# Optimization experiments

Hardware: AMD Instinct MI355X
Metric: run time of the kernel (lower is better)

## Reference

```python
import jax, jax.numpy as jnp
import numpy as np

N = 100000   # nodes
E = 1600000  # edges (avg in-degree 16)
IN, H, C = 128, 128, 40
K = 2        # TAGConv hops (DGL default)


def setup_inputs() -> dict:
    key = jax.random.key(0)
    ks = jax.random.split(key, 7)
    in_feat = jax.random.normal(ks[0], (N, IN), dtype=jnp.float32)
    src = jax.random.randint(ks[1], (E,), 0, N)
    dst = jax.random.randint(ks[2], (E,), 0, N)
    # TAGConv linear: concat of (K+1) hop features -> out
    W1 = jax.random.normal(ks[3], ((K + 1) * IN, H), dtype=jnp.float32) / np.float32(np.sqrt((K + 1) * IN))
    b1 = jnp.zeros((H,), dtype=jnp.float32)
    W2 = jax.random.normal(ks[4], ((K + 1) * H, C), dtype=jnp.float32) / np.float32(np.sqrt((K + 1) * H))
    b2 = jnp.zeros((C,), dtype=jnp.float32)
    return {"in_feat": in_feat, "src": src, "dst": dst,
            "W1": W1, "b1": b1, "W2": W2, "b2": b2}


def _tagconv(x, src, dst, norm, W, b):
    feats = [x]
    h = x
    for _ in range(K):
        h = norm[:, None] * h                               # [N, d]
        h = jax.ops.segment_sum(h[src], dst, num_segments=N)  # SpMM via gather+scatter
        h = norm[:, None] * h
        feats.append(h)
    return jnp.concatenate(feats, axis=-1) @ W + b


def reference(in_feat, src, dst, W1, b1, W2, b2):
    deg = jax.ops.segment_sum(jnp.ones((E,), jnp.float32), dst, num_segments=N)
    norm = jnp.where(deg > 0, deg ** -0.5, 0.0)             # D^{-1/2}, inf -> 0
    h = jax.nn.relu(_tagconv(in_feat, src, dst, norm, W1, b1))
    h = jax.nn.relu(_tagconv(h, src, dst, norm, W2, b2))
    return jnp.mean(h, axis=0, keepdims=True)               # dgl.mean_nodes -> [1, C]
```

## Files before the change

kernel.cpp:

```cpp
#include <hip/hip_runtime.h>

typedef unsigned short u16;
typedef __attribute__((ext_vector_type(8))) short bf16x8;
typedef __attribute__((ext_vector_type(4))) float f32x4;

#define CSR_CHUNK 12288

__device__ inline u16 f2bf(float f) {
    union { float f; unsigned u; } v; v.f = f;
    unsigned r = v.u + 0x7fff + ((v.u >> 16) & 1);
    return (u16)(r >> 16);
}
__device__ inline float bflo(unsigned u) {
    union { unsigned u; float f; } v; v.u = u << 16; return v.f;
}
__device__ inline float bfhi(unsigned u) {
    union { unsigned u; float f; } v; v.u = u & 0xffff0000u; return v.f;
}
__device__ inline float bfs(u16 x) { return bflo((unsigned)x); }
__device__ inline unsigned pk(float lo, float hi) {
    return (unsigned)f2bf(lo) | ((unsigned)f2bf(hi) << 16);
}

__global__ __launch_bounds__(256) void prep_k(
    const float* __restrict__ X, u16* __restrict__ Xb, long n4,
    const float* __restrict__ W1, u16* __restrict__ Wp1,
    const float* __restrict__ W2, u16* __restrict__ Wp2,
    int* __restrict__ bcnt, int nzero) {
    int b = blockIdx.x;
    int t = threadIdx.x;
    if (b < 4) {
        int i = b * 256 + t;
        if (i < nzero) bcnt[i] = 0;
        return;
    }
    b -= 4;
    if (b < 192) {
        int i = b * 256 + t;
        int m = i >> 14, r = i & 16383;
        int jj = r & 7, lane = (r >> 3) & 63, kk = (r >> 9) & 3, tt = r >> 11;
        int k = kk * 32 + (lane >> 4) * 8 + jj;
        int c = tt * 16 + (lane & 15);
        Wp1[i] = f2bf(W1[(size_t)m * 16384 + k * 128 + c]);
        return;
    }
    b -= 192;
    if (b < 64) {
        int i = b * 256 + t;
        int jj = i & 7, lane = (i >> 3) & 63, kk = (i >> 9) & 3, tt = i >> 11;
        int k = kk * 32 + (lane >> 4) * 8 + jj;
        int c = tt * 16 + (lane & 15);
        float v = 0.f;
        if (c < 120) {
            int hop = c / 40, j = c - hop * 40;
            v = W2[(size_t)(hop * 128 + k) * 40 + j];
        }
        Wp2[i] = f2bf(v);
        return;
    }
    b -= 64;
    long i = (long)b * 256 + t;
    if (i >= n4) return;
    float4 v = ((const float4*)X)[i];
    ushort4 o;
    o.x = f2bf(v.x); o.y = f2bf(v.y); o.z = f2bf(v.z); o.w = f2bf(v.w);
    ((ushort4*)Xb)[i] = o;
}

__global__ __launch_bounds__(256) void bucket_cnt_k(
    const int* __restrict__ dst, int* __restrict__ bcnt, int E, int nbuck) {
    __shared__ int hist[1024];
    int e0 = blockIdx.x * CSR_CHUNK;
    int e1 = min(e0 + CSR_CHUNK, E);
    for (int i = threadIdx.x; i < nbuck; i += 256) hist[i] = 0;
    __syncthreads();
    for (int e = e0 + threadIdx.x; e < e1; e += 256)
        atomicAdd(&hist[dst[e] >> 7], 1);
    __syncthreads();
    for (int i = threadIdx.x; i < nbuck; i += 256) {
        int c = hist[i];
        if (c) atomicAdd(&bcnt[i], c);
    }
}

__global__ void bscan_k(const int* __restrict__ bcnt, int* __restrict__ bptr,
                        int* __restrict__ bcur, int nb, int E) {
    __shared__ int lds[256];
    int t = threadIdx.x;
    int base = t * 4;
    int v[4];
    int s = 0;
#pragma unroll
    for (int i = 0; i < 4; ++i) {
        v[i] = s;
        int idx = base + i;
        s += (idx < nb) ? bcnt[idx] : 0;
    }
    int x = s;
    lds[t] = x;
    __syncthreads();
    for (int off = 1; off < 256; off <<= 1) {
        int y = (t >= off) ? lds[t - off] : 0;
        __syncthreads();
        x += y;
        lds[t] = x;
        __syncthreads();
    }
    int toff = x - s;
#pragma unroll
    for (int i = 0; i < 4; ++i) {
        int idx = base + i;
        if (idx < nb) {
            int e0 = toff + v[i];
            bptr[idx] = e0;
            bcur[idx] = e0;
        }
    }
    if (t == 255) bptr[nb] = E;
}

__global__ __launch_bounds__(256) void passB_k(
    const int* __restrict__ src, const int* __restrict__ dst,
    int* __restrict__ bcur, int2* __restrict__ tmp, int E, int nbuck) {
    __shared__ int hist[1024];
    __shared__ int bbase[1024];
    int e0 = blockIdx.x * CSR_CHUNK;
    int e1 = min(e0 + CSR_CHUNK, E);
    for (int i = threadIdx.x; i < nbuck; i += 256) hist[i] = 0;
    __syncthreads();
    for (int e = e0 + threadIdx.x; e < e1; e += 256)
        atomicAdd(&hist[dst[e] >> 7], 1);
    __syncthreads();
    for (int i = threadIdx.x; i < nbuck; i += 256) {
        int c = hist[i];
        bbase[i] = c ? atomicAdd(&bcur[i], c) : 0;
        hist[i] = 0;
    }
    __syncthreads();
    for (int e = e0 + threadIdx.x; e < e1; e += 256) {
        int s = src[e], d = dst[e];
        int b = d >> 7;
        int r = atomicAdd(&hist[b], 1);
        int2 sd; sd.x = s; sd.y = d;
        tmp[bbase[b] + r] = sd;
    }
}

__global__ __launch_bounds__(256) void passC_k(
    const int2* __restrict__ tmp, const int* __restrict__ bptr,
    int* __restrict__ rowptr, float* __restrict__ norm, int* __restrict__ esrc,
    int N, int E) {
    __shared__ int cnt[128];
    __shared__ int sc[128];
    __shared__ int cur[128];
    int b = blockIdx.x, t = threadIdx.x;
    int base = bptr[b], endp = bptr[b + 1];
    int node0 = b << 7;
    int nNodes = min(128, N - node0);

    if (t < 128) cnt[t] = 0;
    __syncthreads();
    for (int i = base + t; i < endp; i += 256)
        atomicAdd(&cnt[tmp[i].y & 127], 1);
    __syncthreads();
    if (t < 128) sc[t] = cnt[t];
    __syncthreads();
    for (int off = 1; off < 128; off <<= 1) {
        int y = 0;
        if (t < 128 && t >= off) y = sc[t - off];
        __syncthreads();
        if (t < 128) sc[t] += y;
        __syncthreads();
    }
    if (t < 128) {
        int ex = sc[t] - cnt[t];
        cur[t] = ex;
        if (t < nNodes) {
            rowptr[node0 + t] = base + ex;
            int d = cnt[t];
            norm[node0 + t] = (d > 0) ? rsqrtf((float)d) : 0.f;
        }
    }
    if (b == gridDim.x - 1 && t == 0) rowptr[N] = E;
    __syncthreads();
    for (int i = base + t; i < endp; i += 256) {
        int2 sd = tmp[i];
        int pos = atomicAdd(&cur[sd.y & 127], 1);
        esrc[base + pos] = sd.x;
    }
}

template <int MODE>
__global__ __launch_bounds__(256, 2) void gemm_mfma_k(
    const u16* __restrict__ Ab, const u16* __restrict__ Wp,
    float* __restrict__ Cf, u16* __restrict__ Cb,
    float* __restrict__ Cf2, u16* __restrict__ Cb2,
    const float* __restrict__ norm, int n, int nStripes) {
    int lane = threadIdx.x & 63;
    int wave = threadIdx.x >> 6;
    int rit = lane & 15;
    int kgrp = lane >> 4;

    bf16x8 bfr[8][4];
    const bf16x8* wp = (const bf16x8*)Wp;
#pragma unroll
    for (int t = 0; t < 8; ++t)
#pragma unroll
        for (int kk = 0; kk < 4; ++kk)
            bfr[t][kk] = wp[(t * 4 + kk) * 64 + lane];

    for (int s = blockIdx.x; s < nStripes; s += gridDim.x) {
        int r0 = s * 64 + wave * 16;
        int ar = min(r0 + rit, n - 1);
        const bf16x8* arow = (const bf16x8*)(Ab + (size_t)ar * 128);
        bf16x8 afr[4];
#pragma unroll
        for (int kk = 0; kk < 4; ++kk) afr[kk] = arow[kk * 4 + kgrp];

        f32x4 acc[8];
#pragma unroll
        for (int t = 0; t < 8; ++t) acc[t] = (f32x4)(0.f);
#pragma unroll
        for (int kk = 0; kk < 4; ++kk)
#pragma unroll
            for (int t = 0; t < 8; ++t)
                acc[t] = __builtin_amdgcn_mfma_f32_16x16x32_bf16(
                    afr[kk], bfr[t][kk], acc[t], 0, 0, 0);

#pragma unroll
        for (int j = 0; j < 4; ++j) {
            int rs = r0 + kgrp * 4 + j;
            if (rs >= n) continue;
            float nr = (MODE == 4) ? 0.f : norm[rs];
#pragma unroll
            for (int t = 0; t < 8; ++t) {
                int c = t * 16 + rit;
                float v = acc[t][j];
                if (MODE == 0) {
                    if (c < 40) Cf[(size_t)rs * 40 + c] = v;
                    else if (c < 80) Cf2[(size_t)rs * 40 + c - 40] = v;
                    else if (c < 120) Cb2[(size_t)rs * 40 + c - 80] = f2bf(v * nr);
                } else if (MODE == 1) {
                    Cb[(size_t)rs * 128 + c] = f2bf(v * nr);
                } else {
                    Cb[(size_t)rs * 128 + c] = f2bf(v);
                }
            }
        }
    }
}

template <int F>
__global__ __launch_bounds__(256) void spmm128_f_k(
    const u16* __restrict__ g, const u16* __restrict__ P,
    const float* __restrict__ bias, u16* __restrict__ outb,
    const float* __restrict__ norm,
    const int* __restrict__ rowptr, const int* __restrict__ esrc, int n) {
    int node = (blockIdx.x * 256 + threadIdx.x) >> 6;
    if (node >= n) return;
    int lane = threadIdx.x & 63;
    int sub = lane >> 4;
    int l16 = lane & 15;
    int beg = rowptr[node], end = rowptr[node + 1];
    float a[8];
#pragma unroll
    for (int j = 0; j < 8; ++j) a[j] = 0.f;

    int e = beg + sub;
    for (; e + 4 < end; e += 8) {
        int s0 = esrc[e], s1 = esrc[e + 4];
        uint4 v0 = *(const uint4*)(g + (size_t)s0 * 128 + l16 * 8);
        uint4 v1 = *(const uint4*)(g + (size_t)s1 * 128 + l16 * 8);
        a[0] += bflo(v0.x); a[1] += bfhi(v0.x);
        a[2] += bflo(v0.y); a[3] += bfhi(v0.y);
        a[4] += bflo(v0.z); a[5] += bfhi(v0.z);
        a[6] += bflo(v0.w); a[7] += bfhi(v0.w);
        a[0] += bflo(v1.x); a[1] += bfhi(v1.x);
        a[2] += bflo(v1.y); a[3] += bfhi(v1.y);
        a[4] += bflo(v1.z); a[5] += bfhi(v1.z);
        a[6] += bflo(v1.w); a[7] += bfhi(v1.w);
    }
    for (; e < end; e += 4) {
        int s = esrc[e];
        uint4 v = *(const uint4*)(g + (size_t)s * 128 + l16 * 8);
        a[0] += bflo(v.x); a[1] += bfhi(v.x);
        a[2] += bflo(v.y); a[3] += bfhi(v.y);
        a[4] += bflo(v.z); a[5] += bfhi(v.z);
        a[6] += bflo(v.w); a[7] += bfhi(v.w);
    }
#pragma unroll
    for (int j = 0; j < 8; ++j) {
        a[j] += __shfl_xor(a[j], 16);
        a[j] += __shfl_xor(a[j], 32);
    }
    if (sub == 0) {
        float nn = norm[node];
        uint4 pv = *(const uint4*)(P + (size_t)node * 128 + l16 * 8);
        float p[8];
        p[0] = bflo(pv.x); p[1] = bfhi(pv.x);
        p[2] = bflo(pv.y); p[3] = bfhi(pv.y);
        p[4] = bflo(pv.z); p[5] = bfhi(pv.z);
        p[6] = bflo(pv.w); p[7] = bfhi(pv.w);
        float r[8];
        if (F == 1) {
#pragma unroll
            for (int j = 0; j < 8; ++j) r[j] = nn * (p[j] + nn * a[j]);
        } else {
            float4 b0 = *(const float4*)(bias + l16 * 8);
            float4 b1v = *(const float4*)(bias + l16 * 8 + 4);
            r[0] = fmaxf(p[0] + nn * a[0] + b0.x, 0.f);
            r[1] = fmaxf(p[1] + nn * a[1] + b0.y, 0.f);
            r[2] = fmaxf(p[2] + nn * a[2] + b0.z, 0.f);
            r[3] = fmaxf(p[3] + nn * a[3] + b0.w, 0.f);
            r[4] = fmaxf(p[4] + nn * a[4] + b1v.x, 0.f);
            r[5] = fmaxf(p[5] + nn * a[5] + b1v.y, 0.f);
            r[6] = fmaxf(p[6] + nn * a[6] + b1v.z, 0.f);
            r[7] = fmaxf(p[7] + nn * a[7] + b1v.w, 0.f);
        }
        uint4 o;
        o.x = pk(r[0], r[1]);
        o.y = pk(r[2], r[3]);
        o.z = pk(r[4], r[5]);
        o.w = pk(r[6], r[7]);
        *(uint4*)(outb + (size_t)node * 128 + l16 * 8) = o;
    }
}

__global__ __launch_bounds__(256) void spmm40_k(
    const u16* __restrict__ Z2b, const float* __restrict__ Z1, u16* __restrict__ u,
    const float* __restrict__ norm, const int* __restrict__ rowptr,
    const int* __restrict__ esrc, int n) {
    int gw = (blockIdx.x * 256 + threadIdx.x) >> 6;
    int lane = threadIdx.x & 63;
    if (gw >= n || lane >= 40) return;
    int beg = rowptr[gw], end = rowptr[gw + 1];
    float a = 0.f;
    int e = beg;
    for (; e + 3 < end; e += 4) {
        int s0 = esrc[e], s1 = esrc[e + 1], s2 = esrc[e + 2], s3 = esrc[e + 3];
        float v0 = bfs(Z2b[(size_t)s0 * 40 + lane]);
        float v1 = bfs(Z2b[(size_t)s1 * 40 + lane]);
        float v2 = bfs(Z2b[(size_t)s2 * 40 + lane]);
        float v3 = bfs(Z2b[(size_t)s3 * 40 + lane]);
        a += (v0 + v1) + (v2 + v3);
    }
    for (; e < end; ++e) a += bfs(Z2b[(size_t)esrc[e] * 40 + lane]);
    float nn = norm[gw];
    u[(size_t)gw * 40 + lane] = f2bf(nn * (Z1[(size_t)gw * 40 + lane] + nn * a));
}

__global__ __launch_bounds__(256) void spmm40_final_k(
    const u16* __restrict__ u, const float* __restrict__ Z0, const float* __restrict__ bias,
    float* __restrict__ partial, const float* __restrict__ norm,
    const int* __restrict__ rowptr, const int* __restrict__ esrc, int n, int nwaves) {
    __shared__ float lds[4][40];
    int wave = threadIdx.x >> 6;
    int lane = threadIdx.x & 63;
    int gw0 = blockIdx.x * 4 + wave;
    float accm = 0.f;
    float bb = (lane < 40) ? bias[lane] : 0.f;
    for (int node = gw0; node < n; node += nwaves) {
        if (lane < 40) {
            int beg = rowptr[node], end = rowptr[node + 1];
            float a = 0.f;
            int e = beg;
            for (; e + 3 < end; e += 4) {
                int s0 = esrc[e], s1 = esrc[e + 1], s2 = esrc[e + 2], s3 = esrc[e + 3];
                float v0 = bfs(u[(size_t)s0 * 40 + lane]);
                float v1 = bfs(u[(size_t)s1 * 40 + lane]);
                float v2 = bfs(u[(size_t)s2 * 40 + lane]);
                float v3 = bfs(u[(size_t)s3 * 40 + lane]);
                a += (v0 + v1) + (v2 + v3);
            }
            for (; e < end; ++e) a += bfs(u[(size_t)esrc[e] * 40 + lane]);
            float r = Z0[(size_t)node * 40 + lane] + norm[node] * a + bb;
            accm += fmaxf(r, 0.f);
        }
    }
    if (lane < 40) lds[wave][lane] = accm;
    __syncthreads();
    if (threadIdx.x < 40) {
        partial[blockIdx.x * 40 + threadIdx.x] =
            lds[0][threadIdx.x] + lds[1][threadIdx.x] + lds[2][threadIdx.x] + lds[3][threadIdx.x];
    }
}

__global__ __launch_bounds__(256) void reduce_mean_k(
    const float* __restrict__ partial, float* __restrict__ out, int nb, float invN) {
    __shared__ float lds[256];
    int c = blockIdx.x, t = threadIdx.x;
    float s = 0.f;
    for (int i = t; i < nb; i += 256) s += partial[(size_t)i * 40 + c];
    lds[t] = s;
    __syncthreads();
    for (int o = 128; o > 0; o >>= 1) {
        if (t < o) lds[t] += lds[t + o];
        __syncthreads();
    }
    if (t == 0) out[c] = lds[0] * invN;
}

extern "C" void kernel_launch(void* const* d_in, const int* in_sizes, int n_in,
                              void* d_out, int out_size, void* d_ws, size_t ws_size,
                              hipStream_t stream) {
    const float* X   = (const float*)d_in[0];
    const int*   src = (const int*)d_in[1];
    const int*   dst = (const int*)d_in[2];
    const float* W1  = (const float*)d_in[3];
    const float* b1  = (const float*)d_in[4];
    const float* W2  = (const float*)d_in[5];
    const float* b2  = (const float*)d_in[6];
    float* out = (float*)d_out;

    const int IN = 128;
    const int N = in_sizes[0] / IN;
    const int E = in_sizes[1];
    const int nb = (N + 127) >> 7;

    char* w = (char*)d_ws;
    size_t off = 0;
    auto alloc = [&](size_t bytes) -> char* {
        char* p = w + off;
        off = (off + bytes + 15) & ~(size_t)15;
        return p;
    };
    float* norm    = (float*)alloc((size_t)N * 4);
    int*   rowptr  = (int*)alloc((size_t)(N + 1) * 4);
    int*   bcnt    = (int*)alloc((size_t)(nb + 1) * 4);
    int*   bptr    = (int*)alloc((size_t)(nb + 1) * 4);
    int*   bcur    = (int*)alloc((size_t)(nb + 1) * 4);
    int*   esrc    = (int*)alloc((size_t)E * 4);
    u16*   Xb      = (u16*)alloc((size_t)N * 128 * 2);
    u16*   h1b     = (u16*)alloc((size_t)N * 128 * 2);
    u16*   g       = (u16*)alloc((size_t)N * 128 * 2);
    u16*   g2      = (u16*)alloc((size_t)N * 128 * 2);
    u16*   Wp1     = (u16*)alloc(3 * 16384 * 2);
    u16*   Wp2     = (u16*)alloc(16384 * 2);
    float* bufF    = (float*)alloc((size_t)N * 128 * 4);
    u16*   ubuf    = (u16*)alloc((size_t)N * 40 * 2);
    float* partial = (float*)alloc(2048 * 40 * 4);

    int2*  tmp = (int2*)bufF;
    u16*   P1b = (u16*)bufF;
    u16*   P0b = (u16*)bufF + (size_t)N * 128;
    float* Z0  = bufF;
    float* Z1  = bufF + (size_t)N * 40;
    u16*   Z2b = (u16*)(bufF + (size_t)2 * N * 40);

    int csr_blocks = (E + CSR_CHUNK - 1) / CSR_CHUNK;
    long n4 = (long)N * 128 / 4;
    int prep_grid = 4 + 192 + 64 + (int)((n4 + 255) / 256);

    prep_k<<<prep_grid, 256, 0, stream>>>(X, Xb, n4, W1, Wp1, W2, Wp2, bcnt, nb);

    bucket_cnt_k<<<csr_blocks, 256, 0, stream>>>(dst, bcnt, E, nb);
    bscan_k<<<1, 256, 0, stream>>>(bcnt, bptr, bcur, nb, E);
    passB_k<<<csr_blocks, 256, 0, stream>>>(src, dst, bcur, tmp, E, nb);
    passC_k<<<nb, 256, 0, stream>>>(tmp, bptr, rowptr, norm, esrc, N, E);

    int nStripes = (N + 63) / 64;
    int gemm_grid = 512;
    int spmm_grid = (N + 3) / 4;

    gemm_mfma_k<1><<<gemm_grid, 256, 0, stream>>>(
        Xb, Wp1 + 2 * 16384, nullptr, g, nullptr, nullptr, norm, N, nStripes);
    gemm_mfma_k<4><<<gemm_grid, 256, 0, stream>>>(
        Xb, Wp1 + 1 * 16384, nullptr, P1b, nullptr, nullptr, norm, N, nStripes);
    gemm_mfma_k<4><<<gemm_grid, 256, 0, stream>>>(
        Xb, Wp1, nullptr, P0b, nullptr, nullptr, norm, N, nStripes);
    spmm128_f_k<1><<<spmm_grid, 256, 0, stream>>>(
        g, P1b, nullptr, g2, norm, rowptr, esrc, N);
    spmm128_f_k<2><<<spmm_grid, 256, 0, stream>>>(
        g2, P0b, b1, h1b, norm, rowptr, esrc, N);

    gemm_mfma_k<0><<<gemm_grid, 256, 0, stream>>>(
        h1b, Wp2, Z0, nullptr, Z1, Z2b, norm, N, nStripes);
    spmm40_k<<<spmm_grid, 256, 0, stream>>>(Z2b, Z1, ubuf, norm, rowptr, esrc, N);
    spmm40_final_k<<<2048, 256, 0, stream>>>(ubuf, Z0, b2, partial, norm, rowptr, esrc, N, 8192);
    reduce_mean_k<<<40, 256, 0, stream>>>(partial, out, 2048, 1.f / (float)N);
}
```

Measured before the change: 427.1 us.

## Slice 128-wide features into column slabs for cache-resident SpMM gathers

Result: slower. 644.0 us (+50.8%).

```diff
diff --git a/kernel.cpp b/kernel.cpp
--- a/kernel.cpp
+++ b/kernel.cpp
@@ -121,7 +121,7 @@
 
 __global__ __launch_bounds__(256) void passB_k(
     const int* __restrict__ src, const int* __restrict__ dst,
-    int* __restrict__ bcur, int2* __restrict__ tmp, int E, int nbuck) {
+    int* __restrict__ bcur, int* __restrict__ tmp, int E, int nbuck) {
     __shared__ int hist[1024];
     __shared__ int bbase[1024];
     int e0 = blockIdx.x * CSR_CHUNK;
@@ -141,13 +141,12 @@
         int s = src[e], d = dst[e];
         int b = d >> 7;
         int r = atomicAdd(&hist[b], 1);
-        int2 sd; sd.x = s; sd.y = d;
-        tmp[bbase[b] + r] = sd;
+        tmp[bbase[b] + r] = (s << 7) | (d & 127);
     }
 }
 
 __global__ __launch_bounds__(256) void passC_k(
-    const int2* __restrict__ tmp, const int* __restrict__ bptr,
+    const int* __restrict__ tmp, const int* __restrict__ bptr,
     int* __restrict__ rowptr, float* __restrict__ norm, int* __restrict__ esrc,
     int N, int E) {
     __shared__ int cnt[128];
@@ -161,7 +160,7 @@
     if (t < 128) cnt[t] = 0;
     __syncthreads();
     for (int i = base + t; i < endp; i += 256)
-        atomicAdd(&cnt[tmp[i].y & 127], 1);
+        atomicAdd(&cnt[tmp[i] & 127], 1);
     __syncthreads();
     if (t < 128) sc[t] = cnt[t];
     __syncthreads();
@@ -184,9 +183,9 @@
     if (b == gridDim.x - 1 && t == 0) rowptr[N] = E;
     __syncthreads();
     for (int i = base + t; i < endp; i += 256) {
-        int2 sd = tmp[i];
-        int pos = atomicAdd(&cur[sd.y & 127], 1);
-        esrc[base + pos] = sd.x;
+        int p = tmp[i];
+        int pos = atomicAdd(&cur[p & 127], 1);
+        esrc[base + pos] = p >> 7;
     }
 }
 
@@ -241,9 +240,9 @@
                     else if (c < 80) Cf2[(size_t)rs * 40 + c - 40] = v;
                     else if (c < 120) Cb2[(size_t)rs * 40 + c - 80] = f2bf(v * nr);
                 } else if (MODE == 1) {
-                    Cb[(size_t)rs * 128 + c] = f2bf(v * nr);
+                    Cb[(((size_t)t * n + rs) << 4) + rit] = f2bf(v * nr);
                 } else {
-                    Cb[(size_t)rs * 128 + c] = f2bf(v);
+                    Cb[(((size_t)t * n + rs) << 4) + rit] = f2bf(v);
                 }
             }
         }
@@ -251,78 +250,70 @@
 }
 
 template <int F>
-__global__ __launch_bounds__(256) void spmm128_f_k(
+__global__ __launch_bounds__(256) void spmm128_sl_k(
     const u16* __restrict__ g, const u16* __restrict__ P,
     const float* __restrict__ bias, u16* __restrict__ outb,
     const float* __restrict__ norm,
     const int* __restrict__ rowptr, const int* __restrict__ esrc, int n) {
-    int node = (blockIdx.x * 256 + threadIdx.x) >> 6;
-    if (node >= n) return;
+    int sl = blockIdx.x & 7;
+    int wave = threadIdx.x >> 6;
     int lane = threadIdx.x & 63;
-    int sub = lane >> 4;
-    int l16 = lane & 15;
-    int beg = rowptr[node], end = rowptr[node + 1];
-    float a[8];
-#pragma unroll
-    for (int j = 0; j < 8; ++j) a[j] = 0.f;
-
-    int e = beg + sub;
-    for (; e + 4 < end; e += 8) {
-        int s0 = esrc[e], s1 = esrc[e + 4];
-        uint4 v0 = *(const uint4*)(g + (size_t)s0 * 128 + l16 * 8);
-        uint4 v1 = *(const uint4*)(g + (size_t)s1 * 128 + l16 * 8);
-        a[0] += bflo(v0.x); a[1] += bfhi(v0.x);
-        a[2] += bflo(v0.y); a[3] += bfhi(v0.y);
-        a[4] += bflo(v0.z); a[5] += bfhi(v0.z);
-        a[6] += bflo(v0.w); a[7] += bfhi(v0.w);
-        a[0] += bflo(v1.x); a[1] += bfhi(v1.x);
-        a[2] += bflo(v1.y); a[3] += bfhi(v1.y);
-        a[4] += bflo(v1.z); a[5] += bfhi(v1.z);
-        a[6] += bflo(v1.w); a[7] += bfhi(v1.w);
-    }
-    for (; e < end; e += 4) {
-        int s = esrc[e];
-        uint4 v = *(const uint4*)(g + (size_t)s * 128 + l16 * 8);
-        a[0] += bflo(v.x); a[1] += bfhi(v.x);
-        a[2] += bflo(v.y); a[3] += bfhi(v.y);
-        a[4] += bflo(v.z); a[5] += bfhi(v.z);
-        a[6] += bflo(v.w); a[7] += bfhi(v.w);
-    }
-#pragma unroll
-    for (int j = 0; j < 8; ++j) {
-        a[j] += __shfl_xor(a[j], 16);
-        a[j] += __shfl_xor(a[j], 32);
-    }
-    if (sub == 0) {
-        float nn = norm[node];
-        uint4 pv = *(const uint4*)(P + (size_t)node * 128 + l16 * 8);
-        float p[8];
-        p[0] = bflo(pv.x); p[1] = bfhi(pv.x);
-        p[2] = bflo(pv.y); p[3] = bfhi(pv.y);
-        p[4] = bflo(pv.z); p[5] = bfhi(pv.z);
-        p[6] = bflo(pv.w); p[7] = bfhi(pv.w);
-        float r[8];
-        if (F == 1) {
-#pragma unroll
-            for (int j = 0; j < 8; ++j) r[j] = nn * (p[j] + nn * a[j]);
-        } else {
-            float4 b0 = *(const float4*)(bias + l16 * 8);
-            float4 b1v = *(const float4*)(bias + l16 * 8 + 4);
-            r[0] = fmaxf(p[0] + nn * a[0] + b0.x, 0.f);
-            r[1] = fmaxf(p[1] + nn * a[1] + b0.y, 0.f);
-            r[2] = fmaxf(p[2] + nn * a[2] + b0.z, 0.f);
-            r[3] = fmaxf(p[3] + nn * a[3] + b0.w, 0.f);
-            r[4] = fmaxf(p[4] + nn * a[4] + b1v.x, 0.f);
-            r[5] = fmaxf(p[5] + nn * a[5] + b1v.y, 0.f);
-            r[6] = fmaxf(p[6] + nn * a[6] + b1v.z, 0.f);
-            r[7] = fmaxf(p[7] + nn * a[7] + b1v.w, 0.f);
-        }
-        uint4 o;
-        o.x = pk(r[0], r[1]);
-        o.y = pk(r[2], r[3]);
-        o.z = pk(r[4], r[5]);
-        o.w = pk(r[6], r[7]);
-        *(uint4*)(outb + (size_t)node * 128 + l16 * 8) = o;
+    int el = lane >> 2;
+    int cl = lane & 3;
+    int nb0 = ((blockIdx.x >> 3) * 4 + wave) * 8;
+    if (nb0 >= n) return;
+    const u16* tab = g + ((size_t)sl * n << 4);
+    const u16* Pt  = P + ((size_t)sl * n << 4);
+    int cbase = sl * 16 + cl * 4;
+    float4 bv;
+    if (F == 2) bv = *(const float4*)(bias + cbase);
+
+#pragma unroll
+    for (int i = 0; i < 8; ++i) {
+        int node = nb0 + i;
+        if (node < n) {
+            int beg = rowptr[node], end = rowptr[node + 1];
+            float a0 = 0.f, a1 = 0.f, a2 = 0.f, a3 = 0.f;
+            for (int e = beg + el; e < end; e += 16) {
+                int s = esrc[e];
+                uint2 v = *(const uint2*)(tab + ((size_t)s << 4) + cl * 4);
+                a0 += bflo(v.x); a1 += bfhi(v.x);
+                a2 += bflo(v.y); a3 += bfhi(v.y);
+            }
+            a0 += __shfl_xor(a0, 4);  a1 += __shfl_xor(a1, 4);
+            a2 += __shfl_xor(a2, 4);  a3 += __shfl_xor(a3, 4);
+            a0 += __shfl_xor(a0, 8);  a1 += __shfl_xor(a1, 8);
+            a2 += __shfl_xor(a2, 8);  a3 += __shfl_xor(a3, 8);
+            a0 += __shfl_xor(a0, 16); a1 += __shfl_xor(a1, 16);
+            a2 += __shfl_xor(a2, 16); a3 += __shfl_xor(a3, 16);
+            a0 += __shfl_xor(a0, 32); a1 += __shfl_xor(a1, 32);
+            a2 += __shfl_xor(a2, 32); a3 += __shfl_xor(a3, 32);
+            if (el == 0) {
+                float nn = norm[node];
+                uint2 pv = *(const uint2*)(Pt + ((size_t)node << 4) + cl * 4);
+                float p0 = bflo(pv.x), p1 = bfhi(pv.x);
+                float p2 = bflo(pv.y), p3 = bfhi(pv.y);
+                float r0, r1, r2, r3;
+                if (F == 1) {
+                    r0 = nn * (p0 + nn * a0);
+                    r1 = nn * (p1 + nn * a1);
+                    r2 = nn * (p2 + nn * a2);
+                    r3 = nn * (p3 + nn * a3);
+                } else {
+                    r0 = fmaxf(p0 + nn * a0 + bv.x, 0.f);
+                    r1 = fmaxf(p1 + nn * a1 + bv.y, 0.f);
+                    r2 = fmaxf(p2 + nn * a2 + bv.z, 0.f);
+                    r3 = fmaxf(p3 + nn * a3 + bv.w, 0.f);
+                }
+                uint2 o;
+                o.x = pk(r0, r1);
+                o.y = pk(r2, r3);
+                if (F == 1)
+                    *(uint2*)(outb + ((size_t)sl * n << 4) + ((size_t)node << 4) + cl * 4) = o;
+                else
+                    *(uint2*)(outb + (size_t)node * 128 + cbase) = o;
+            }
+        }
     }
 }
 
@@ -440,7 +431,7 @@
     u16*   ubuf    = (u16*)alloc((size_t)N * 40 * 2);
     float* partial = (float*)alloc(2048 * 40 * 4);
 
-    int2*  tmp = (int2*)bufF;
+    int*   tmp = (int*)bufF;
     u16*   P1b = (u16*)bufF;
     u16*   P0b = (u16*)bufF + (size_t)N * 128;
     float* Z0  = bufF;
@@ -461,6 +452,7 @@
     int nStripes = (N + 63) / 64;
     int gemm_grid = 512;
     int spmm_grid = (N + 3) / 4;
+    int spmm_sl_grid = 8 * ((N + 31) / 32);
 
     gemm_mfma_k<1><<<gemm_grid, 256, 0, stream>>>(
         Xb, Wp1 + 2 * 16384, nullptr, g, nullptr, nullptr, norm, N, nStripes);
@@ -468,9 +460,9 @@
         Xb, Wp1 + 1 * 16384, nullptr, P1b, nullptr, nullptr, norm, N, nStripes);
     gemm_mfma_k<4><<<gemm_grid, 256, 0, stream>>>(
         Xb, Wp1, nullptr, P0b, nullptr, nullptr, norm, N, nStripes);
-    spmm128_f_k<1><<<spmm_grid, 256, 0, stream>>>(
+    spmm128_sl_k<1><<<spmm_sl_grid, 256, 0, stream>>>(
         g, P1b, nullptr, g2, norm, rowptr, esrc, N);
-    spmm128_f_k<2><<<spmm_grid, 256, 0, stream>>>(
+    spmm128_sl_k<2><<<spmm_sl_grid, 256, 0, stream>>>(
         g2, P0b, b1, h1b, norm, rowptr, esrc, N);
 
     gemm_mfma_k<0><<<gemm_grid, 256, 0, stream>>>(
```
